# Kernel tuning notes

Hardware: AMD Instinct MI355X
Metric: run time of the kernel (lower is better)

## Reference

```python
import jax, jax.numpy as jnp
import numpy as np

B, N, D, H, NW = 16, 400, 256, 8, 4
DH = D // H
EPS_LN = 1e-5

def _layer_norm(x, g, b):
    m = jnp.mean(x, axis=-1, keepdims=True)
    v = jnp.mean((x - m) ** 2, axis=-1, keepdims=True)
    return (x - m) / jnp.sqrt(v + EPS_LN) * g + b

def setup_inputs() -> dict:
    key = jax.random.key(0)
    ks = jax.random.split(key, 10)
    p = lambda k, shape: (jax.random.normal(k, shape, jnp.float32) * 0.02)
    return {
        'x': jax.random.normal(ks[0], (B, N, D), jnp.float32),
        'attention_weights': jax.random.normal(ks[1], (B, NW, N, N), jnp.float32),
        'Wq': p(ks[2], (D, D)), 'bq': jnp.zeros((D,), jnp.float32),
        'Wk': p(ks[3], (D, D)), 'bk': jnp.zeros((D,), jnp.float32),
        'Wv': p(ks[4], (D, D)), 'bv': jnp.zeros((D,), jnp.float32),
        'Wo': p(ks[5], (D, D)), 'bo': jnp.zeros((D,), jnp.float32),
        'g1': jnp.ones((D,), jnp.float32), 'beta1': jnp.zeros((D,), jnp.float32),
        'W1': p(ks[6], (4 * D, D)), 'b1': jnp.zeros((4 * D,), jnp.float32),
        'W2': p(ks[7], (D, 4 * D)), 'b2': jnp.zeros((D,), jnp.float32),
        'g2': jnp.ones((D,), jnp.float32), 'beta2': jnp.zeros((D,), jnp.float32),
    }

def reference(x, attention_weights, Wq, bq, Wk, bk, Wv, bv, Wo, bo,
              g1, beta1, W1, b1, W2, b2, g2, beta2):
    b, n, d = x.shape
    # QKV projections, split heads: [B, H, N, DH]
    q = (x @ Wq.T + bq).reshape(b, n, H, DH).transpose(0, 2, 1, 3)
    k = (x @ Wk.T + bk).reshape(b, n, H, DH).transpose(0, 2, 1, 3)
    v = (x @ Wv.T + bv).reshape(b, n, H, DH).transpose(0, 2, 1, 3)
    qk = jnp.einsum('bhnd,bhmd->bhnm', q, k) / np.sqrt(DH)  # [B,H,N,N]
    # signed attention averaged over the NW per-sample weight matrices
    nw = attention_weights.shape[1]
    scores = jnp.zeros_like(qk)
    for i in range(nw):  # small fixed count, not a data dim
        w = attention_weights[:, i][:, None, :, :]  # [B,1,N,N]
        s = qk * w
        e = jnp.exp(jnp.abs(s))
        scores = scores + jnp.sign(s) * e / (jnp.sum(e, axis=-1, keepdims=True) + 1e-10)
    scores = scores / nw
    attn_out = jnp.einsum('bhnm,bhmd->bhnd', scores, v)
    attn_out = attn_out.transpose(0, 2, 1, 3).reshape(b, n, d)
    attn_out = attn_out @ Wo.T + bo
    h = _layer_norm(x + attn_out, g1, beta1)
    ffn = jax.nn.relu(h @ W1.T + b1) @ W2.T + b2
    y = _layer_norm(h + ffn, g2, beta2)
    return (y, scores)
```

## Files before the change

### kernel.cpp

```cpp
#include <hip/hip_runtime.h>
#include <hip/hip_fp16.h>

typedef unsigned int uint32;

#define B_ 16
#define N_ 400
#define D_ 256
#define H_ 8
#define DH_ 32
#define NW_ 4

#if __has_builtin(__builtin_amdgcn_exp2f)
#define EXP2(x) __builtin_amdgcn_exp2f(x)
#else
#define EXP2(x) exp2f(x)
#endif

#define QK_SCL 0.2550348f

using bf16x8 = __attribute__((ext_vector_type(8))) short;
using f16x8  = __attribute__((ext_vector_type(8))) _Float16;
using f32x4  = __attribute__((ext_vector_type(4))) float;

__device__ __forceinline__ ushort f2b(float f) {
  uint32 u = __float_as_uint(f);
  uint32 r = (u + 0x7fffu + ((u >> 16) & 1u)) >> 16;
  return (ushort)r;
}

__global__ __launch_bounds__(256) void convert_kernel(
    const float* __restrict__ x,  const float* __restrict__ wq,
    const float* __restrict__ wk, const float* __restrict__ wv,
    const float* __restrict__ wo, const float* __restrict__ w1,
    const float* __restrict__ w2,
    ushort* __restrict__ xb,  ushort* __restrict__ wqb,
    ushort* __restrict__ wkb, ushort* __restrict__ wvb,
    ushort* __restrict__ wob, ushort* __restrict__ w1b,
    ushort* __restrict__ w2b) {
  int gid = blockIdx.x * 256 + threadIdx.x;
  const float* src; ushort* dst;
  if      (gid < 409600) { src = x;  dst = xb;  }
  else if ((gid -= 409600) < 16384) { src = wq; dst = wqb; }
  else if ((gid -= 16384) < 16384)  { src = wk; dst = wkb; }
  else if ((gid -= 16384) < 16384)  { src = wv; dst = wvb; }
  else if ((gid -= 16384) < 16384)  { src = wo; dst = wob; }
  else if ((gid -= 16384) < 65536)  { src = w1; dst = w1b; }
  else { gid -= 65536; src = w2; dst = w2b; }
  float4 f = ((const float4*)src)[gid];
  ushort4 u;
  u.x = f2b(f.x); u.y = f2b(f.y); u.z = f2b(f.z); u.w = f2b(f.w);
  *(ushort4*)&dst[(size_t)gid * 4] = u;
}

template <int RELU, int RESID, int OUT_F32, int OUT_BF16>
__global__ __launch_bounds__(256) void gemm_bt(
    const ushort* __restrict__ A, const ushort* __restrict__ W,
    const float* __restrict__ bias, const float* __restrict__ resid,
    float* __restrict__ outf, ushort* __restrict__ outb,
    int M, int N, int K) {
  __shared__ __align__(16) ushort As[2][64 * 40];
  __shared__ __align__(16) ushort Ws[2][64 * 40];
  int t = threadIdx.x;
  int l = t & 63, w = t >> 6;
  int n0 = blockIdx.x * 64, m0 = blockIdx.y * 64;
  int srow = t >> 2, sc = (t & 3) * 8;
  int lrow = l & 15, lk = (l >> 4) * 8;

  const uint4* ag = (const uint4*)&A[(size_t)(m0 + srow) * K + sc];
  const uint4* wg = (const uint4*)&W[(size_t)(n0 + srow) * K + sc];
  uint4 ar = ag[0], wr = wg[0];
  int nk = K >> 5;

  f32x4 acc[4];
#pragma unroll
  for (int nt = 0; nt < 4; nt++) acc[nt] = {0.f, 0.f, 0.f, 0.f};

  for (int kk = 0; kk < nk; kk++) {
    int cur = kk & 1;
    *(uint4*)&As[cur][srow * 40 + sc] = ar;
    *(uint4*)&Ws[cur][srow * 40 + sc] = wr;
    if (kk + 1 < nk) { ar = ag[(size_t)(kk + 1) * 4]; wr = wg[(size_t)(kk + 1) * 4]; }
    __syncthreads();
    bf16x8 af = *(const bf16x8*)&As[cur][(16 * w + lrow) * 40 + lk];
#pragma unroll
    for (int nt = 0; nt < 4; nt++) {
      bf16x8 bf = *(const bf16x8*)&Ws[cur][(nt * 16 + lrow) * 40 + lk];
      acc[nt] = __builtin_amdgcn_mfma_f32_16x16x32_bf16(af, bf, acc[nt], 0, 0, 0);
    }
  }

#pragma unroll
  for (int nt = 0; nt < 4; nt++) {
    int n = n0 + nt * 16 + lrow;
    float bv = bias[n];
#pragma unroll
    for (int r = 0; r < 4; r++) {
      int m = m0 + 16 * w + (l >> 4) * 4 + r;
      float v = acc[nt][r] + bv;
      if (RELU)  v = fmaxf(v, 0.f);
      if (RESID) v += resid[(size_t)m * N + n];
      if (OUT_F32)  outf[(size_t)m * N + n] = v;
      if (OUT_BF16) outb[(size_t)m * N + n] = f2b(v);
    }
  }
}

__global__ __launch_bounds__(256) void qkv_gemm(
    const ushort* __restrict__ xb, const ushort* __restrict__ wq,
    const ushort* __restrict__ wk, const ushort* __restrict__ wv,
    const float* __restrict__ bq, const float* __restrict__ bk,
    const float* __restrict__ bv,
    _Float16* __restrict__ qh, _Float16* __restrict__ kh,
    _Float16* __restrict__ vt) {
  __shared__ __align__(16) ushort As[2][64 * 40];
  __shared__ __align__(16) ushort Ws[2][64 * 40];
  int z = blockIdx.z;
  const ushort* W = (z == 0) ? wq : (z == 1) ? wk : wv;
  const float* bias = (z == 0) ? bq : (z == 1) ? bk : bv;

  int t = threadIdx.x;
  int l = t & 63, w = t >> 6;
  int n0 = blockIdx.x * 64, m0 = blockIdx.y * 64;
  int srow = t >> 2, sc = (t & 3) * 8;
  int lrow = l & 15, lk = (l >> 4) * 8;

  const uint4* ag = (const uint4*)&xb[(size_t)(m0 + srow) * 256 + sc];
  const uint4* wg = (const uint4*)&W[(size_t)(n0 + srow) * 256 + sc];
  uint4 ar = ag[0], wr = wg[0];

  f32x4 acc[4];
#pragma unroll
  for (int nt = 0; nt < 4; nt++) acc[nt] = {0.f, 0.f, 0.f, 0.f};

  for (int kk = 0; kk < 8; kk++) {
    int cur = kk & 1;
    *(uint4*)&As[cur][srow * 40 + sc] = ar;
    *(uint4*)&Ws[cur][srow * 40 + sc] = wr;
    if (kk + 1 < 8) { ar = ag[(kk + 1) * 4]; wr = wg[(kk + 1) * 4]; }
    __syncthreads();
    bf16x8 af = *(const bf16x8*)&As[cur][(16 * w + lrow) * 40 + lk];
#pragma unroll
    for (int nt = 0; nt < 4; nt++) {
      bf16x8 bf = *(const bf16x8*)&Ws[cur][(nt * 16 + lrow) * 40 + lk];
      acc[nt] = __builtin_amdgcn_mfma_f32_16x16x32_bf16(af, bf, acc[nt], 0, 0, 0);
    }
  }

  int mb = m0 + 16 * w + (l >> 4) * 4;
  int bb = mb / 400;
  int mi = mb - bb * 400;
#pragma unroll
  for (int nt = 0; nt < 4; nt++) {
    int n = n0 + nt * 16 + lrow;
    float bvv = bias[n];
    if (z < 2) {
      _Float16* out = z ? kh : qh;
      float scl = z ? 1.f : QK_SCL;
      int hh = n >> 5, dd = n & 31;
      _Float16* dst = out + (((size_t)(bb * 8 + hh)) * 400 + mi) * 32 + dd;
#pragma unroll
      for (int r = 0; r < 4; r++)
        dst[(size_t)r * 32] = (_Float16)((acc[nt][r] + bvv) * scl);
    } else {
      _Float16 h4[4];
#pragma unroll
      for (int r = 0; r < 4; r++) h4[r] = (_Float16)(acc[nt][r] + bvv);
      *(uint2*)&vt[((size_t)bb * 256 + n) * 400 + mi] = *(uint2*)h4;
    }
  }
}

#define SP 416

__global__ __launch_bounds__(256) void attn_kernel(
    const _Float16* __restrict__ qh, const _Float16* __restrict__ kh,
    const _Float16* __restrict__ vt, const float* __restrict__ aw,
    float* __restrict__ scores, ushort* __restrict__ attnb) {
  __shared__ __align__(16) char smem[16 * SP * 2 + 256];
  __half* S = (__half*)smem;
  float* zin = (float*)(smem + 16 * SP * 2);

  int id = blockIdx.x;
  int c = ((id >> 6) << 3) | (id & 7);
  int hh = (id >> 3) & 7;
  int b = c / 25;
  int n0 = (c - b * 25) * 16;

  int t = threadIdx.x;
  int w = t >> 6, l = t & 63;
  int lq = l >> 4, lr = l & 15;

  {
    const _Float16* qbase = qh + (((size_t)(b * 8 + hh)) * 400 + n0) * 32;
    const _Float16* kbase = kh + ((size_t)(b * 8 + hh)) * 400 * 32;
    f16x8 af = *(const f16x8*)(qbase + lr * 32 + lq * 8);
    for (int mt = w; mt < 25; mt += 4) {
      f16x8 bf = *(const f16x8*)(kbase + (size_t)(mt * 16 + lr) * 32 + lq * 8);
      f32x4 cc = {0.f, 0.f, 0.f, 0.f};
      cc = __builtin_amdgcn_mfma_f32_16x16x32_f16(af, bf, cc, 0, 0, 0);
#pragma unroll
      for (int r = 0; r < 4; r++)
        S[(lq * 4 + r) * SP + mt * 16 + lr] = __float2half(cc[r]);
    }
  }
  __syncthreads();

  {
    int r = t >> 2, p = t & 3;
    int i = r >> 4, n = r & 15;
    const float* wrow = aw + (((size_t)(b * 4 + i)) * 400 + n0 + n) * 400;
    const __half* srow = S + n * SP;
    float z = 0.f;
    for (int m = p * 4; m < 400; m += 16) {
      float4 wv = *(const float4*)(wrow + m);
      float2 f0 = __half22float2(*(const __half2*)(srow + m));
      float2 f1 = __half22float2(*(const __half2*)(srow + m + 2));
      z += EXP2(fabsf(f0.x * wv.x)) + EXP2(fabsf(f0.y * wv.y)) +
           EXP2(fabsf(f1.x * wv.z)) + EXP2(fabsf(f1.y * wv.w));
    }
    z += __shfl_xor(z, 1);
    z += __shfl_xor(z, 2);
    if (p == 0) zin[r] = 0.25f / (z + 1e-10f);
  }
  __syncthreads();

  {
    int n = t >> 4, p = t & 15;
    float zz[4] = {zin[n], zin[16 + n], zin[32 + n], zin[48 + n]};
    __half* srow = S + n * SP;
    const float* awn = aw + (((size_t)(b * 4)) * 400 + n0 + n) * 400;
    float* scout = scores + (((size_t)(b * 8 + hh)) * 400 + n0 + n) * 400;
    for (int m = p * 4; m < 448; m += 64) {
      if (m < 400) {
        float2 f0 = __half22float2(*(const __half2*)(srow + m));
        float2 f1 = __half22float2(*(const __half2*)(srow + m + 2));
        float q0 = f0.x, q1 = f0.y, q2 = f1.x, q3 = f1.y;
        float s0 = 0.f, s1 = 0.f, s2 = 0.f, s3 = 0.f;
#pragma unroll
        for (int i = 0; i < 4; i++) {
          float4 wv = *(const float4*)(awn + (size_t)i * 160000 + m);
          float t0 = q0 * wv.x; s0 += copysignf(EXP2(fabsf(t0)) * zz[i], t0);
          float t1 = q1 * wv.y; s1 += copysignf(EXP2(fabsf(t1)) * zz[i], t1);
          float t2 = q2 * wv.z; s2 += copysignf(EXP2(fabsf(t2)) * zz[i], t2);
          float t3 = q3 * wv.w; s3 += copysignf(EXP2(fabsf(t3)) * zz[i], t3);
        }
        float4 o = {s0, s1, s2, s3};
        *(float4*)(scout + m) = o;
        __half h4[4] = {__float2half(s0), __float2half(s1),
                        __float2half(s2), __float2half(s3)};
        *(uint2*)(srow + m) = *(uint2*)h4;
      } else if (m < 416) {
        uint2 zero = {0u, 0u};
        *(uint2*)(srow + m) = zero;
      }
    }
  }
  __syncthreads();

  const _Float16* vbase = vt + (((size_t)b) * 256 + hh * 32) * 400;
  f32x4 a0 = {0.f, 0.f, 0.f, 0.f}, a1 = {0.f, 0.f, 0.f, 0.f};
  const _Float16* Sh = (const _Float16*)S;
  for (int c2 = w; c2 < 13; c2 += 4) {
    f16x8 sf = *(const f16x8*)(Sh + lr * SP + c2 * 32 + lq * 8);
    f16x8 v0 = *(const f16x8*)(vbase + (size_t)lr * 400 + c2 * 32 + lq * 8);
    f16x8 v1 = *(const f16x8*)(vbase + (size_t)(16 + lr) * 400 + c2 * 32 + lq * 8);
    a0 = __builtin_amdgcn_mfma_f32_16x16x32_f16(sf, v0, a0, 0, 0, 0);
    a1 = __builtin_amdgcn_mfma_f32_16x16x32_f16(sf, v1, a1, 0, 0, 0);
  }
  __syncthreads();
  float* Of = (float*)smem;
#pragma unroll
  for (int r = 0; r < 4; r++) {
    Of[(w * 16 + lq * 4 + r) * 32 + lr] = a0[r];
    Of[(w * 16 + lq * 4 + r) * 32 + 16 + lr] = a1[r];
  }
  __syncthreads();
  for (int o = t; o < 512; o += 256) {
    int n = o >> 5, d = o & 31;
    float s = Of[n * 32 + d] + Of[512 + n * 32 + d] +
              Of[1024 + n * 32 + d] + Of[1536 + n * 32 + d];
    attnb[((size_t)(b * 400 + n0 + n)) * 256 + hh * 32 + d] = f2b(s);
  }
}

__global__ __launch_bounds__(256) void ln_kernel(
    const float* __restrict__ src, const float* __restrict__ g,
    const float* __restrict__ be, float* __restrict__ outf,
    ushort* __restrict__ outb) {
  int row = blockIdx.x, t = threadIdx.x;
  float v = src[(size_t)row * 256 + t];
  __shared__ float red[4];
  float s = v;
#pragma unroll
  for (int o = 32; o > 0; o >>= 1) s += __shfl_down(s, o, 64);
  if ((t & 63) == 0) red[t >> 6] = s;
  __syncthreads();
  float mean = (red[0] + red[1] + red[2] + red[3]) * (1.f / 256.f);
  __syncthreads();
  float d = v - mean;
  s = d * d;
#pragma unroll
  for (int o = 32; o > 0; o >>= 1) s += __shfl_down(s, o, 64);
  if ((t & 63) == 0) red[t >> 6] = s;
  __syncthreads();
  float var = (red[0] + red[1] + red[2] + red[3]) * (1.f / 256.f);
  float y = d * rsqrtf(var + 1e-5f) * g[t] + be[t];
  outf[(size_t)row * 256 + t] = y;
  if (outb) outb[(size_t)row * 256 + t] = f2b(y);
}

extern "C" void kernel_launch(void* const* d_in, const int* in_sizes, int n_in,
                              void* d_out, int out_size, void* d_ws,
                              size_t ws_size, hipStream_t stream) {
  const float* x   = (const float*)d_in[0];
  const float* aw  = (const float*)d_in[1];
  const float* Wq  = (const float*)d_in[2];
  const float* bq  = (const float*)d_in[3];
  const float* Wk  = (const float*)d_in[4];
  const float* bk  = (const float*)d_in[5];
  const float* Wv  = (const float*)d_in[6];
  const float* bv  = (const float*)d_in[7];
  const float* Wo  = (const float*)d_in[8];
  const float* bo  = (const float*)d_in[9];
  const float* g1  = (const float*)d_in[10];
  const float* be1 = (const float*)d_in[11];
  const float* W1  = (const float*)d_in[12];
  const float* b1  = (const float*)d_in[13];
  const float* W2  = (const float*)d_in[14];
  const float* b2  = (const float*)d_in[15];
  const float* g2  = (const float*)d_in[16];
  const float* be2 = (const float*)d_in[17];

  if (ws_size < 34340864) return;

  char* ws = (char*)d_ws;
  ushort*   xb    = (ushort*)(ws + 0);
  ushort*   wqb   = (ushort*)(ws + 3276800);
  ushort*   wkb   = (ushort*)(ws + 3407872);
  ushort*   wvb   = (ushort*)(ws + 3538944);
  ushort*   wob   = (ushort*)(ws + 3670016);
  ushort*   w1b   = (ushort*)(ws + 3801088);
  ushort*   w2b   = (ushort*)(ws + 4325376);
  _Float16* qhb   = (_Float16*)(ws + 4849664);
  _Float16* khb   = (_Float16*)(ws + 8126464);
  _Float16* vtb   = (_Float16*)(ws + 11403264);
  ushort*   attnb = (ushort*)(ws + 14680064);
  float*    ao    = (float*)(ws + 17956864);
  float*    hbuf  = (float*)(ws + 24510464);
  ushort*   hb    = (ushort*)(ws + 31064064);
  ushort*   ffn1b = (ushort*)qhb;
  float*    ffn2  = ao;

  float* yout   = (float*)d_out;
  float* scores = yout + 1638400;

  convert_kernel<<<2368, 256, 0, stream>>>(x, Wq, Wk, Wv, Wo, W1, W2,
                                           xb, wqb, wkb, wvb, wob, w1b, w2b);
  qkv_gemm<<<dim3(4, 100, 3), 256, 0, stream>>>(
      xb, wqb, wkb, wvb, bq, bk, bv, qhb, khb, vtb);
  attn_kernel<<<3200, 256, 0, stream>>>(qhb, khb, vtb, aw, scores, attnb);
  gemm_bt<0, 1, 1, 0><<<dim3(4, 100), 256, 0, stream>>>(
      attnb, wob, bo, x, ao, nullptr, 6400, 256, 256);
  ln_kernel<<<6400, 256, 0, stream>>>(ao, g1, be1, hbuf, hb);
  gemm_bt<1, 0, 0, 1><<<dim3(16, 100), 256, 0, stream>>>(
      hb, w1b, b1, nullptr, nullptr, ffn1b, 6400, 1024, 256);
  gemm_bt<0, 1, 1, 0><<<dim3(4, 100), 256, 0, stream>>>(
      ffn1b, w2b, b2, hbuf, ffn2, nullptr, 6400, 256, 1024);
  ln_kernel<<<6400, 256, 0, stream>>>(ffn2, g2, be2, yout, nullptr);
}
```

Before: 272.5 us.

## Fuse softmax normalizer and score passes into single wave-per-row pass

The two-phase score computation is merged. Previously one pass summed the exp terms into shared memory and a second pass reread the attention weights and recomputed the exponentials. Now each wave owns four rows and computes the exps once, keeping them as fp16 in registers. It reduces each row sum with wave shuffles, then normalizes and writes the outputs. This halves the global reads of attention_weights, removes one barrier and halves the exp work. In exchange it adds a six-step shuffle reduction per row and weight, and rounds the intermediate exps to fp16 before normalization, which adds precision loss.

```diff
diff --git a/kernel.cpp b/kernel.cpp
--- a/kernel.cpp
+++ b/kernel.cpp
@@ -20,6 +20,7 @@
 
 using bf16x8 = __attribute__((ext_vector_type(8))) short;
 using f16x8  = __attribute__((ext_vector_type(8))) _Float16;
+using f16x4  = __attribute__((ext_vector_type(4))) _Float16;
 using f32x4  = __attribute__((ext_vector_type(4))) float;
 
 __device__ __forceinline__ ushort f2b(float f) {
@@ -176,9 +177,8 @@
     const _Float16* __restrict__ qh, const _Float16* __restrict__ kh,
     const _Float16* __restrict__ vt, const float* __restrict__ aw,
     float* __restrict__ scores, ushort* __restrict__ attnb) {
-  __shared__ __align__(16) char smem[16 * SP * 2 + 256];
+  __shared__ __align__(16) char smem[16 * SP * 2];
   __half* S = (__half*)smem;
-  float* zin = (float*)(smem + 16 * SP * 2);
 
   int id = blockIdx.x;
   int c = ((id >> 6) << 3) | (id & 7);
@@ -206,52 +206,79 @@
   __syncthreads();
 
   {
-    int r = t >> 2, p = t & 3;
-    int i = r >> 4, n = r & 15;
-    const float* wrow = aw + (((size_t)(b * 4 + i)) * 400 + n0 + n) * 400;
-    const __half* srow = S + n * SP;
-    float z = 0.f;
-    for (int m = p * 4; m < 400; m += 16) {
-      float4 wv = *(const float4*)(wrow + m);
-      float2 f0 = __half22float2(*(const __half2*)(srow + m));
-      float2 f1 = __half22float2(*(const __half2*)(srow + m + 2));
-      z += EXP2(fabsf(f0.x * wv.x)) + EXP2(fabsf(f0.y * wv.y)) +
-           EXP2(fabsf(f1.x * wv.z)) + EXP2(fabsf(f1.y * wv.w));
-    }
-    z += __shfl_xor(z, 1);
-    z += __shfl_xor(z, 2);
-    if (p == 0) zin[r] = 0.25f / (z + 1e-10f);
-  }
-  __syncthreads();
-
-  {
-    int n = t >> 4, p = t & 15;
-    float zz[4] = {zin[n], zin[16 + n], zin[32 + n], zin[48 + n]};
-    __half* srow = S + n * SP;
-    const float* awn = aw + (((size_t)(b * 4)) * 400 + n0 + n) * 400;
-    float* scout = scores + (((size_t)(b * 8 + hh)) * 400 + n0 + n) * 400;
-    for (int m = p * 4; m < 448; m += 64) {
-      if (m < 400) {
-        float2 f0 = __half22float2(*(const __half2*)(srow + m));
-        float2 f1 = __half22float2(*(const __half2*)(srow + m + 2));
-        float q0 = f0.x, q1 = f0.y, q2 = f1.x, q3 = f1.y;
-        float s0 = 0.f, s1 = 0.f, s2 = 0.f, s3 = 0.f;
-#pragma unroll
-        for (int i = 0; i < 4; i++) {
-          float4 wv = *(const float4*)(awn + (size_t)i * 160000 + m);
-          float t0 = q0 * wv.x; s0 += copysignf(EXP2(fabsf(t0)) * zz[i], t0);
-          float t1 = q1 * wv.y; s1 += copysignf(EXP2(fabsf(t1)) * zz[i], t1);
-          float t2 = q2 * wv.z; s2 += copysignf(EXP2(fabsf(t2)) * zz[i], t2);
-          float t3 = q3 * wv.w; s3 += copysignf(EXP2(fabsf(t3)) * zz[i], t3);
+    _Float16* Sh16 = (_Float16*)S;
+    const float* awb = aw + (((size_t)(b * 4)) * 400 + n0) * 400;
+    float* scb = scores + (((size_t)(b * 8 + hh)) * 400 + n0) * 400;
+    int m0 = l * 4, m1 = 256 + l * 4;
+    bool act = (l < 36);
+#pragma unroll 1
+    for (int nn = 0; nn < 4; nn++) {
+      int n = w * 4 + nn;
+      _Float16* srow = Sh16 + (size_t)n * SP;
+      f16x4 s0 = *(const f16x4*)(srow + m0);
+      f16x4 s1; s1[0] = s1[1] = s1[2] = s1[3] = (_Float16)0.f;
+      if (act) s1 = *(const f16x4*)(srow + m1);
+      float q0[4], q1[4];
+#pragma unroll
+      for (int j = 0; j < 4; j++) { q0[j] = (float)s0[j]; q1[j] = (float)s1[j]; }
+      f16x4 e0[4], e1[4];
+      float zinv[4];
+#pragma unroll
+      for (int i = 0; i < 4; i++) {
+        const float* awn = awb + (size_t)i * 160000 + (size_t)n * 400;
+        float4 a0 = *(const float4*)(awn + m0);
+        float z = 0.f;
+#pragma unroll
+        for (int j = 0; j < 4; j++) {
+          float tt = q0[j] * ((const float*)&a0)[j];
+          float ef = EXP2(fabsf(tt));
+          z += ef;
+          e0[i][j] = (_Float16)copysignf(ef, tt);
         }
-        float4 o = {s0, s1, s2, s3};
-        *(float4*)(scout + m) = o;
-        __half h4[4] = {__float2half(s0), __float2half(s1),
-                        __float2half(s2), __float2half(s3)};
-        *(uint2*)(srow + m) = *(uint2*)h4;
-      } else if (m < 416) {
-        uint2 zero = {0u, 0u};
-        *(uint2*)(srow + m) = zero;
+        if (act) {
+          float4 a1 = *(const float4*)(awn + m1);
+#pragma unroll
+          for (int j = 0; j < 4; j++) {
+            float tt = q1[j] * ((const float*)&a1)[j];
+            float ef = EXP2(fabsf(tt));
+            z += ef;
+            e1[i][j] = (_Float16)copysignf(ef, tt);
+          }
+        } else {
+          e1[i][0] = e1[i][1] = e1[i][2] = e1[i][3] = (_Float16)0.f;
+        }
+        z += __shfl_xor(z, 1);
+        z += __shfl_xor(z, 2);
+        z += __shfl_xor(z, 4);
+        z += __shfl_xor(z, 8);
+        z += __shfl_xor(z, 16);
+        z += __shfl_xor(z, 32);
+        zinv[i] = 0.25f / (z + 1e-10f);
+      }
+      float o0[4] = {0.f, 0.f, 0.f, 0.f}, o1[4] = {0.f, 0.f, 0.f, 0.f};
+#pragma unroll
+      for (int i = 0; i < 4; i++) {
+#pragma unroll
+        for (int j = 0; j < 4; j++) {
+          o0[j] += (float)e0[i][j] * zinv[i];
+          o1[j] += (float)e1[i][j] * zinv[i];
+        }
+      }
+      float* scout = scb + (size_t)n * 400;
+      *(float4*)(scout + m0) = *(float4*)o0;
+      f16x4 h0;
+#pragma unroll
+      for (int j = 0; j < 4; j++) h0[j] = (_Float16)o0[j];
+      *(f16x4*)(srow + m0) = h0;
+      if (act) {
+        *(float4*)(scout + m1) = *(float4*)o1;
+        f16x4 h1;
+#pragma unroll
+        for (int j = 0; j < 4; j++) h1[j] = (_Float16)o1[j];
+        *(f16x4*)(srow + m1) = h1;
+      } else if (l < 40) {
+        f16x4 hz; hz[0] = hz[1] = hz[2] = hz[3] = (_Float16)0.f;
+        *(f16x4*)(srow + m1) = hz;
       }
     }
   }
```

Result: slower. 283.1 us (+3.9%).
